# Optimization experiments

Measured on AMD Instinct MI355X. Metric: run time of the kernel, lower is better.

The kernel has to match this reference:

```python
import jax, jax.numpy as jnp
import numpy as np
from jax import lax

B, TENC, TMEL = 32, 512, 400
E, H, A, P, M, F, K = 512, 512, 512, 256, 128, 32, 31


def setup_inputs() -> dict:
    key = jax.random.key(0)
    ks = jax.random.split(key, 20)
    def rn(i, shape, fan_in):
        return jax.random.normal(ks[i], shape, jnp.float32) / np.float32(np.sqrt(fan_in))
    return dict(
        enc_outputs=jax.random.normal(ks[0], (B, TENC, 2 * E), jnp.float32),
        mel_spec_true=jax.random.normal(ks[1], (B, TMEL, M), jnp.float32),
        text_lens=jax.random.randint(ks[2], (B,), 0, TENC),
        mel_spec_lens=jax.random.randint(ks[3], (B,), 0, TMEL),
        max_text_len=TENC,
        pre_w1=rn(4, (M, P), M), pre_w2=rn(5, (P, P), P),
        attn_wi=rn(6, (P + E, 3 * H), P + E), attn_wh=rn(7, (H, 3 * H), H),
        attn_bi=jnp.zeros((3 * H,), jnp.float32), attn_bh=jnp.zeros((3 * H,), jnp.float32),
        q_w=rn(8, (H, A), H), k_w=rn(9, (2 * E, A), 2 * E),
        score_w=rn(10, (A, 1), A), score_b=jnp.zeros((1,), jnp.float32),
        loc_conv_w=rn(11, (F, 2, K), 2 * K), loc_w=rn(12, (F, A), F), loc_b=jnp.zeros((A,), jnp.float32),
        out_wi=rn(13, (A + H, 3 * H), A + H), out_wh=rn(14, (H, 3 * H), H),
        out_bi=jnp.zeros((3 * H,), jnp.float32), out_bh=jnp.zeros((3 * H,), jnp.float32),
        dec_w=rn(15, (H + A, M), H + A), dec_b=jnp.zeros((M,), jnp.float32),
        gate_w=rn(16, (H + A, 1), H + A), gate_b=jnp.zeros((1,), jnp.float32),
    )


def _gru_step(x, h, wi, wh, bi, bh):
    # single-step torch nn.GRU cell; gate order r, z, n
    gi = x @ wi + bi
    gh = h @ wh + bh
    ir, iz, inn = jnp.split(gi, 3, axis=-1)
    hr, hz, hn = jnp.split(gh, 3, axis=-1)
    r = jax.nn.sigmoid(ir + hr)
    z = jax.nn.sigmoid(iz + hz)
    n = jnp.tanh(inn + r * hn)
    return (1.0 - z) * n + z * h


def reference(enc_outputs, mel_spec_true, text_lens, mel_spec_lens, max_text_len,
              pre_w1, pre_w2, attn_wi, attn_wh, attn_bi, attn_bh,
              q_w, k_w, score_w, score_b, loc_conv_w, loc_w, loc_b,
              out_wi, out_wh, out_bi, out_bh, dec_w, dec_b, gate_w, gate_b):
    Bsz, Tenc, _ = enc_outputs.shape
    Tmel = mel_spec_true.shape[1]
    Hd = attn_wh.shape[0]
    Ad = k_w.shape[1]
    pad = (loc_conv_w.shape[2] - 1) // 2

    keys_p = enc_outputs @ k_w                                # [B,Tenc,A]
    enc_mask = jnp.arange(Tenc)[None, :] > text_lens[:, None]  # True = masked (t > len)

    def prenet(x):  # dropout disabled for determinism
        return jax.nn.relu(jax.nn.relu(x @ pre_w1) @ pre_w2)

    dec_in0 = prenet(jnp.zeros((Bsz, mel_spec_true.shape[2]), enc_outputs.dtype))
    carry0 = (jnp.zeros((Bsz, Hd), jnp.float32), jnp.zeros((Bsz, Hd), jnp.float32),
              jnp.zeros((Bsz, Tenc), jnp.float32), jnp.zeros((Bsz, Tenc), jnp.float32),
              jnp.zeros((Bsz, Ad), jnp.float32), dec_in0)

    def step(carry, _):
        h_attn, h_out, att_w, att_cum, ctx, dec_in = carry
        h_attn = _gru_step(jnp.concatenate([dec_in, ctx], -1), h_attn, attn_wi, attn_wh, attn_bi, attn_bh)
        loc_in = jnp.stack([att_w, att_cum], axis=1)           # [B,2,Tenc]
        loc = lax.conv_general_dilated(loc_in, loc_conv_w, (1,), [(pad, pad)],
                                       dimension_numbers=('NCH', 'OIH', 'NCH'))  # [B,F,Tenc]
        loc = jnp.swapaxes(loc, 1, 2) @ loc_w + loc_b          # [B,Tenc,A]
        q = (h_attn @ q_w)[:, None, :]                         # [B,1,A]
        s = (jnp.tanh(q + keys_p + loc) @ score_w + score_b)[..., 0]  # [B,Tenc]
        s = jnp.where(enc_mask, -jnp.inf, s)
        att_w = jax.nn.softmax(s, axis=1)
        ctx = jnp.einsum('bt,bta->ba', att_w, keys_p)
        att_cum = att_cum + att_w
        h_out = _gru_step(jnp.concatenate([h_attn, ctx], -1), h_out, out_wi, out_wh, out_bi, out_bh)
        att_h = jnp.concatenate([h_out, ctx], -1)
        mel = att_h @ dec_w + dec_b                            # [B,M]
        stop = (att_h @ gate_w + gate_b)[:, 0]                 # [B]
        dec_in = prenet(mel)                                   # teacher_force_ratio = 0
        return (h_attn, h_out, att_w, att_cum, ctx, dec_in), (mel, stop, att_w)

    _, (mels, gates, attns) = lax.scan(step, carry0, None, length=Tmel)
    mels = jnp.swapaxes(mels, 0, 1)    # [B,Tmel,M]
    gates = jnp.swapaxes(gates, 0, 1)  # [B,Tmel]
    attns = jnp.swapaxes(attns, 0, 1)  # [B,Tmel,Tenc]
    mel_mask = jnp.arange(Tmel)[None, :] > mel_spec_lens[:, None]
    masked_mel = jnp.where(mel_mask[:, :, None], 0.0, mels)
    masked_gate = jnp.where(mel_mask, 1000.0, gates)
    return masked_mel, masked_gate, attns, mel_mask
```

## Files before the change

### kernel.cpp

```cpp
#include <hip/hip_runtime.h>
#include <hip/hip_fp16.h>
#include <math.h>

#define NBLK 256
#define NTHR 1024

__device__ __forceinline__ float fast_rcp(float x) {
#if __has_builtin(__builtin_amdgcn_rcpf)
  return __builtin_amdgcn_rcpf(x);
#else
  return 1.f / x;
#endif
}
__device__ __forceinline__ float fast_sigmoid(float x) { return fast_rcp(1.f + __expf(-x)); }
__device__ __forceinline__ float fast_tanh(float x) { return 1.f - 2.f * fast_rcp(1.f + __expf(2.f * x)); }

union HU2 { unsigned int u; __half2 h; };
union HU4 { uint4 u; __half2 h[4]; };
__device__ __forceinline__ float2 cvt2(unsigned int u) { HU2 t; t.u = u; return __half22float2(t.h); }

__device__ __forceinline__ void sta(float* p, float v) {
  __hip_atomic_store(p, v, __ATOMIC_RELAXED, __HIP_MEMORY_SCOPE_AGENT);
}
__device__ __forceinline__ float lda(const float* p) {
  return __hip_atomic_load(p, __ATOMIC_RELAXED, __HIP_MEMORY_SCOPE_AGENT);
}
__device__ __forceinline__ int ldai(const int* p) {
  return __hip_atomic_load(p, __ATOMIC_RELAXED, __HIP_MEMORY_SCOPE_AGENT);
}
__device__ __forceinline__ void ntst(float* p, float v) { __builtin_nontemporal_store(v, p); }

struct Params {
  const float *enc, *pre_w1, *pre_w2, *attn_bi, *attn_bh;
  const float *q_w, *k_w, *score_w, *score_b, *conv_w, *loc_w, *loc_b;
  const float *out_bi, *out_bh, *dec_b, *gate_b;
  const float *attn_wi, *attn_wh, *out_wi, *out_wh, *dec_w, *gate_w;
  const int *text_lens, *mel_lens;
  __half *hkeys, *gw1T, *gw2T, *decT, *pre1T, *pre2T, *gateh, *locwh, *qwT;
  float *hA, *hO, *attw, *attcum, *decin, *ebuf, *zpart, *ctxacc, *ctxacc2, *stateZ;
  int *done, *zdone, *done2, *hAdone;
  unsigned *barc;
  float *out_mel, *out_gate, *out_attn, *out_mask;
};

__global__ __launch_bounds__(512) void k_keys(Params p) {
  __shared__ float sA[16][132];
  __shared__ float sB[16][68];
  int tid = threadIdx.x;
  int row0 = blockIdx.x * 128, col0 = blockIdx.y * 64;
  float acc[4][4] = {};
  int r = tid >> 2, kq = tid & 3;
  int tx = tid & 15, ty = tid >> 4;
  for (int k0 = 0; k0 < 1024; k0 += 16) {
    __syncthreads();
    float4 a4 = *(const float4*)(p.enc + (size_t)(row0 + r) * 1024 + k0 + kq * 4);
    sA[kq * 4 + 0][r] = a4.x; sA[kq * 4 + 1][r] = a4.y;
    sA[kq * 4 + 2][r] = a4.z; sA[kq * 4 + 3][r] = a4.w;
    if (tid < 256) {
      int kb = tid >> 4, nb = (tid & 15) * 4;
      float4 b4 = *(const float4*)(p.k_w + (size_t)(k0 + kb) * 512 + col0 + nb);
      sB[kb][nb + 0] = b4.x; sB[kb][nb + 1] = b4.y;
      sB[kb][nb + 2] = b4.z; sB[kb][nb + 3] = b4.w;
    }
    __syncthreads();
#pragma unroll
    for (int k = 0; k < 16; k++) {
      float ar[4], br[4];
#pragma unroll
      for (int i = 0; i < 4; i++) { ar[i] = sA[k][ty * 4 + i]; br[i] = sB[k][tx * 4 + i]; }
#pragma unroll
      for (int i = 0; i < 4; i++)
#pragma unroll
        for (int j = 0; j < 4; j++) acc[i][j] = fmaf(ar[i], br[j], acc[i][j]);
    }
  }
#pragma unroll
  for (int i = 0; i < 4; i++)
#pragma unroll
    for (int j = 0; j < 4; j++)
      p.hkeys[(size_t)(row0 + ty * 4 + i) * 512 + col0 + tx * 4 + j] = __float2half(acc[i][j]);
}

__global__ __launch_bounds__(256) void k_repack(Params p) {
  const int gsz = gridDim.x * 256;
  const int t0 = blockIdx.x * 256 + threadIdx.x;
  for (int i = t0; i < 1280 * 512; i += gsz) {
    int r = i >> 9, u = i & 511;
    const float* src = (r < 768) ? p.attn_wi + (size_t)r * 1536 : p.attn_wh + (size_t)(r - 768) * 1536;
    __half2* d = (__half2*)(p.gw1T + ((size_t)i << 2));
    d[0] = __halves2half2(__float2half(src[u]), __float2half(src[512 + u]));
    d[1] = __halves2half2(__float2half(src[1024 + u]), __float2half(0.f));
  }
  for (int i = t0; i < 1536 * 512; i += gsz) {
    int r = i >> 9, u = i & 511;
    const float* src = (r < 1024) ? p.out_wi + (size_t)r * 1536 : p.out_wh + (size_t)(r - 1024) * 1536;
    __half2* d = (__half2*)(p.gw2T + ((size_t)i << 2));
    d[0] = __halves2half2(__float2half(src[u]), __float2half(src[512 + u]));
    d[1] = __halves2half2(__float2half(src[1024 + u]), __float2half(0.f));
  }
  for (int i = t0; i < 512 * 512; i += gsz) {
    int k = i >> 9, a = i & 511;
    p.qwT[(size_t)a * 512 + k] = __float2half(p.q_w[(size_t)k * 512 + a]);
  }
  for (int i = t0; i < 1024 * 128; i += gsz) {
    int k = i >> 7, m = i & 127;
    p.decT[(size_t)m * 1024 + k] = __float2half(p.dec_w[(size_t)k * 128 + m]);
  }
  for (int i = t0; i < 1024; i += gsz) p.gateh[i] = __float2half(p.gate_w[i]);
  for (int i = t0; i < 16384; i += gsz) p.locwh[i] = __float2half(p.loc_w[i]);
  for (int i = t0; i < 128 * 256; i += gsz) {
    int m = i >> 8, pc = i & 255;
    p.pre1T[(size_t)pc * 128 + m] = __float2half(p.pre_w1[(size_t)m * 256 + pc]);
  }
  for (int i = t0; i < 256 * 256; i += gsz) {
    int k = i >> 8, pc = i & 255;
    p.pre2T[(size_t)pc * 256 + k] = __float2half(p.pre_w2[(size_t)k * 256 + pc]);
  }
  for (int i = t0; i < 106496; i += gsz) p.stateZ[i] = 0.f;
  for (int i = t0; i < 16384; i += gsz) p.ctxacc[i] = 0.f;
  for (int i = t0; i < 16384; i += gsz) p.ctxacc2[i] = 0.f;
  for (int i = t0; i < 512; i += gsz) p.barc[i] = 0u;
  for (int i = t0; i < 2048; i += gsz) p.zdone[i] = 0;
  for (int i = t0; i < 12800; i += gsz) {
    int b = i / 400, t = i - b * 400;
    p.out_mask[i] = (t > p.mel_lens[b]) ? 1.f : 0.f;
  }
}

struct SMemMega {
  __half keysL[64 * 512];
  float ctxL[4][512];
  float invZ[4];
  union {
    struct { float x[4][1544]; float4 part4[16][64]; } gr;
    struct { float locS[64][33]; float aw[94]; float ac[94]; float hA_s[512]; float qS[512];
             float qpart[2][512]; float cpred[8][512]; float eS[64]; } s3;
    struct { float xh[1024]; float red[1024]; float mel[128]; float p1[256]; } s6;
  } u;
};

__device__ __forceinline__ void gchunk(const uint2* __restrict__ w,
                                       const float* __restrict__ x, int ks,
                                       int j0, int j1,
                                       float& a0, float& a1, float& a2) {
#pragma unroll 8
  for (int j = j0; j < j1; ++j) {
    uint2 wv = w[(size_t)j << 13];
    float xv = x[ks + (j << 4)];
    float2 f0 = cvt2(wv.x);
    float nf = cvt2(wv.y).x;
    a0 = fmaf(xv, f0.x, a0);
    a1 = fmaf(xv, f0.y, a1);
    a2 = fmaf(xv, nf, a2);
  }
}

__global__ __launch_bounds__(NTHR) void mega(Params p) {
  __shared__ SMemMega sm;
  const int blk = blockIdx.x, tid = threadIdx.x;
  const int ug = blk & 31, bg = blk >> 5, b0 = bg * 4;
  const int bS = blk & 31, t8 = blk >> 5, t0g = t8 << 6;

  const int u_ = tid & 15, b2_ = (tid >> 4) & 3, ks_ = tid >> 6;
  const int uG_ = (ug << 4) + u_;
  const uint2* w1 = (const uint2*)p.gw1T + ((size_t)ks_ << 9) + uG_;
  const uint2* w2 = (const uint2*)p.gw2T + ((size_t)ks_ << 9) + uG_;

  {
    const uint4* src = (const uint4*)(p.hkeys + (((size_t)(bS << 9) + t0g) << 9));
    uint4* dst = (uint4*)sm.keysL;
    for (int i = tid; i < 4096; i += NTHR) dst[i] = src[i];
    for (int i = tid; i < 2048; i += NTHR) sm.ctxL[i >> 9][i & 511] = 0.f;
  }
  __syncthreads();

  float g1r = 0.f, g1z = 0.f, g1ni = 0.f, g1nh = 0.f;

#pragma clang loop unroll(disable)
  for (int step = 0; step < 400; step++) {
    const int par = step & 1;
    float* hA_prev = p.hA + par * 16384;
    float* hA_next = p.hA + (par ^ 1) * 16384;
    float* hO_prev = p.hO + par * 16384;
    float* hO_next = p.hO + (par ^ 1) * 16384;
    float* cCur = par ? p.ctxacc2 : p.ctxacc;
    float* cNxt = par ? p.ctxacc : p.ctxacc2;

    {
      if (step > 0) {
        if (tid < 4) {
          while (ldai(&p.done2[(b0 + tid) * 16]) < 4 * step)
            __builtin_amdgcn_s_sleep(2);
        }
        __syncthreads();
      }
      for (int i = tid; i < 1024; i += NTHR)
        sm.u.gr.x[i >> 8][i & 255] = lda(&p.decin[((b0 + (i >> 8)) << 8) + (i & 255)]);
      __syncthreads();
      gchunk(w1, &sm.u.gr.x[b2_][0], ks_, 0, 16, g1r, g1z, g1ni);
      sm.u.gr.part4[ks_][(u_ << 2) + b2_] = make_float4(g1r, g1z, g1ni, g1nh);
      __syncthreads();
      if (tid < 64) {
        int uu = tid >> 2, bb2 = tid & 3;
        float4 s = make_float4(0.f, 0.f, 0.f, 0.f);
#pragma unroll
        for (int l = 0; l < 16; l++) {
          float4 v = sm.u.gr.part4[l][(uu << 2) + bb2];
          s.x += v.x; s.y += v.y; s.z += v.z; s.w += v.w;
        }
        int uGf = (ug << 4) + uu;
        float r = fast_sigmoid(s.x + p.attn_bi[uGf] + p.attn_bh[uGf]);
        float z = fast_sigmoid(s.y + p.attn_bi[512 + uGf] + p.attn_bh[512 + uGf]);
        float n = fast_tanh(s.z + p.attn_bi[1024 + uGf] + r * (s.w + p.attn_bh[1024 + uGf]));
        float hv = lda(&hA_prev[((b0 + bb2) << 9) + uGf]);
        sta(&hA_next[((b0 + bb2) << 9) + uGf], (1.f - z) * n + z * hv);
      }
      asm volatile("s_waitcnt vmcnt(0)" ::: "memory");
      if (tid < 4) atomicAdd(&p.hAdone[(b0 + tid) * 16], 1);
    }

    {
      if (tid == 0) {
        while (ldai(&p.hAdone[bS * 16]) < 32 * (step + 1))
          __builtin_amdgcn_s_sleep(2);
      }
      __syncthreads();
      if (t8 == 0) {
        for (int i = tid; i < 512; i += NTHR) sta(&cNxt[(bS << 9) + i], 0.f);
      }
      const int tlen = p.text_lens[bS];
      for (int j = tid; j < 94; j += NTHR) {
        int pp = t0g - 15 + j;
        bool ok = (unsigned)pp < 512u;
        sm.u.s3.aw[j] = ok ? lda(&p.attw[(bS << 9) + pp]) : 0.f;
        sm.u.s3.ac[j] = ok ? lda(&p.attcum[(bS << 9) + pp]) : 0.f;
      }
      if (tid < 512) sm.u.s3.hA_s[tid] = lda(&hA_next[(bS << 9) + tid]);
      __syncthreads();
      for (int i = tid; i < 2048; i += NTHR) {
        int tt = i >> 5, f = i & 31;
        const float* w0 = p.conv_w + f * 62;
        float a = 0.f;
#pragma unroll
        for (int k = 0; k < 31; k++)
          a = fmaf(w0[k], sm.u.s3.aw[tt + k], fmaf(w0[31 + k], sm.u.s3.ac[tt + k], a));
        sm.u.s3.locS[tt][f] = a;
      }
      {
        int a = tid & 511, ks = tid >> 9;
        const HU4* qp = (const HU4*)(p.qwT + (size_t)a * 512 + ks * 256);
        float q0 = 0.f, q1 = 0.f;
#pragma unroll 4
        for (int it = 0; it < 32; it++) {
          HU4 raw = qp[it];
          int kb = ks * 256 + it * 8;
#pragma unroll
          for (int h2 = 0; h2 < 4; h2++) {
            float2 w = __half22float2(raw.h[h2]);
            q0 = fmaf(sm.u.s3.hA_s[kb + h2 * 2], w.x, q0);
            q1 = fmaf(sm.u.s3.hA_s[kb + h2 * 2 + 1], w.y, q1);
          }
        }
        sm.u.s3.qpart[ks][a] = q0 + q1;
      }
      __syncthreads();
      if (tid < 512)
        sm.u.s3.qS[tid] = sm.u.s3.qpart[0][tid] + sm.u.s3.qpart[1][tid] + p.loc_b[tid];
      __syncthreads();
      const int lane = tid & 63, wv = tid >> 6;
      float acc[4][8];
      float4 qA = *(const float4*)&sm.u.s3.qS[lane * 8];
      float4 qB = *(const float4*)&sm.u.s3.qS[lane * 8 + 4];
#pragma unroll
      for (int j = 0; j < 4; j++) {
        int tL = wv * 4 + j;
        HU4 raw; raw.u = *(const uint4*)&sm.keysL[tL * 512 + lane * 8];
        float2 k0 = __half22float2(raw.h[0]), k1 = __half22float2(raw.h[1]);
        float2 k2 = __half22float2(raw.h[2]), k3 = __half22float2(raw.h[3]);
        acc[j][0] = qA.x + k0.x; acc[j][1] = qA.y + k0.y;
        acc[j][2] = qA.z + k1.x; acc[j][3] = qA.w + k1.y;
        acc[j][4] = qB.x + k2.x; acc[j][5] = qB.y + k2.y;
        acc[j][6] = qB.z + k3.x; acc[j][7] = qB.w + k3.y;
      }
#pragma unroll 4
      for (int f = 0; f < 32; f++) {
        HU4 rw; rw.u = *(const uint4*)(p.locwh + (size_t)f * 512 + lane * 8);
        float2 w0 = __half22float2(rw.h[0]), w1 = __half22float2(rw.h[1]);
        float2 w2 = __half22float2(rw.h[2]), w3 = __half22float2(rw.h[3]);
#pragma unroll
        for (int j = 0; j < 4; j++) {
          float lf = sm.u.s3.locS[wv * 4 + j][f];
          acc[j][0] = fmaf(lf, w0.x, acc[j][0]); acc[j][1] = fmaf(lf, w0.y, acc[j][1]);
          acc[j][2] = fmaf(lf, w1.x, acc[j][2]); acc[j][3] = fmaf(lf, w1.y, acc[j][3]);
          acc[j][4] = fmaf(lf, w2.x, acc[j][4]); acc[j][5] = fmaf(lf, w2.y, acc[j][5]);
          acc[j][6] = fmaf(lf, w3.x, acc[j][6]); acc[j][7] = fmaf(lf, w3.y, acc[j][7]);
        }
      }
      float4 sA = *(const float4*)(p.score_w + lane * 8);
      float4 sB = *(const float4*)(p.score_w + lane * 8 + 4);
      float sbias = p.score_b[0];
      float e_reg[4];
#pragma unroll
      for (int j = 0; j < 4; j++) {
        float pv = fast_tanh(acc[j][0]) * sA.x + fast_tanh(acc[j][1]) * sA.y +
                   fast_tanh(acc[j][2]) * sA.z + fast_tanh(acc[j][3]) * sA.w +
                   fast_tanh(acc[j][4]) * sB.x + fast_tanh(acc[j][5]) * sB.y +
                   fast_tanh(acc[j][6]) * sB.z + fast_tanh(acc[j][7]) * sB.w;
#pragma unroll
        for (int off = 32; off > 0; off >>= 1) pv += __shfl_xor(pv, off, 64);
        int t = t0g + wv * 4 + j;
        e_reg[j] = (t > tlen) ? 0.f : __expf(pv + sbias);
      }
      if (lane == 0) {
#pragma unroll
        for (int j = 0; j < 4; j++) sm.u.s3.eS[wv * 4 + j] = e_reg[j];
      }
      float cp[8] = {0.f, 0.f, 0.f, 0.f, 0.f, 0.f, 0.f, 0.f};
#pragma unroll
      for (int j = 0; j < 4; j++) {
        int tL = wv * 4 + j;
        HU4 raw; raw.u = *(const uint4*)&sm.keysL[tL * 512 + lane * 8];
        float2 k0 = __half22float2(raw.h[0]), k1 = __half22float2(raw.h[1]);
        float2 k2 = __half22float2(raw.h[2]), k3 = __half22float2(raw.h[3]);
        float e = e_reg[j];
        cp[0] = fmaf(e, k0.x, cp[0]); cp[1] = fmaf(e, k0.y, cp[1]);
        cp[2] = fmaf(e, k1.x, cp[2]); cp[3] = fmaf(e, k1.y, cp[3]);
        cp[4] = fmaf(e, k2.x, cp[4]); cp[5] = fmaf(e, k2.y, cp[5]);
        cp[6] = fmaf(e, k3.x, cp[6]); cp[7] = fmaf(e, k3.y, cp[7]);
      }
      __syncthreads();
      if (wv < 8) {
        float4* r0 = (float4*)&sm.u.s3.cpred[wv][lane * 8];
        r0[0] = make_float4(cp[0], cp[1], cp[2], cp[3]);
        r0[1] = make_float4(cp[4], cp[5], cp[6], cp[7]);
      }
      __syncthreads();
      if (wv >= 8) {
        float* r0 = &sm.u.s3.cpred[wv - 8][lane * 8];
#pragma unroll
        for (int i = 0; i < 8; i++) r0[i] += cp[i];
      }
      __syncthreads();
      if (tid < 512) {
        float s = 0.f;
#pragma unroll
        for (int j = 0; j < 8; j++) s += sm.u.s3.cpred[j][tid];
        atomicAdd(&cCur[(bS << 9) + tid], s);
      }
      if (tid < 64) {
        float e = sm.u.s3.eS[tid];
        sta(&p.ebuf[(bS << 9) + t0g + tid], e);
        float z = e;
#pragma unroll
        for (int off = 32; off > 0; off >>= 1) z += __shfl_xor(z, off, 64);
        if (tid == 0) sta(&p.zpart[bS * 8 + t8], z);
      }
      if (tid < 512 && (tid & 63) == 0) {
        asm volatile("s_waitcnt vmcnt(0)" ::: "memory");
        atomicAdd(&p.zdone[bS * 16], 1);
      }
    }

    {
      if (tid < 4) {
        while (ldai(&p.zdone[(b0 + tid) * 16]) < 64 * (step + 1))
          __builtin_amdgcn_s_sleep(2);
        float Z = 0.f;
#pragma unroll
        for (int j = 0; j < 8; j++) Z += lda(&p.zpart[(b0 + tid) * 8 + j]);
        sm.invZ[tid] = fast_rcp(Z);
      }
      __syncthreads();
      for (int i = tid; i < 2048; i += NTHR) {
        int b2 = i >> 9, a = i & 511;
        sm.ctxL[b2][a] = lda(&cCur[((b0 + b2) << 9) + a]) * sm.invZ[b2];
      }
      if (ug == 0) {
        for (int i = tid; i < 2048; i += NTHR) {
          int b2 = i >> 9, t = i & 511;
          int bb = b0 + b2;
          float v = lda(&p.ebuf[(bb << 9) + t]) * sm.invZ[b2];
          sta(&p.attw[(bb << 9) + t], v);
          float oc = lda(&p.attcum[(bb << 9) + t]);
          sta(&p.attcum[(bb << 9) + t], oc + v);
          ntst(&p.out_attn[(size_t)bb * 204800 + (size_t)step * 512 + t], v);
        }
      }
      __syncthreads();
      for (int i = tid; i < 2048; i += NTHR) {
        int b2 = i >> 9, a = i & 511;
        sm.u.gr.x[b2][a] = lda(&hA_next[((b0 + b2) << 9) + a]);
      }
      for (int i = tid; i < 2048; i += NTHR) {
        int b2 = i >> 9, a = i & 511;
        sm.u.gr.x[b2][512 + a] = sm.ctxL[b2][a];
      }
      for (int i = tid; i < 2048; i += NTHR) {
        int b2 = i >> 9, a = i & 511;
        sm.u.gr.x[b2][1024 + a] = lda(&hO_prev[((b0 + b2) << 9) + a]);
      }
      __syncthreads();
      {
        float r2 = 0.f, z2 = 0.f, ni2 = 0.f, nh2 = 0.f;
        gchunk(w2, &sm.u.gr.x[b2_][0], ks_, 0, 64, r2, z2, ni2);
        gchunk(w2, &sm.u.gr.x[b2_][0], ks_, 64, 96, r2, z2, nh2);
        sm.u.gr.part4[ks_][(u_ << 2) + b2_] = make_float4(r2, z2, ni2, nh2);
      }
      __syncthreads();
      if (tid < 64) {
        int uu = tid >> 2, bb2 = tid & 3;
        float4 s = make_float4(0.f, 0.f, 0.f, 0.f);
#pragma unroll
        for (int l = 0; l < 16; l++) {
          float4 v = sm.u.gr.part4[l][(uu << 2) + bb2];
          s.x += v.x; s.y += v.y; s.z += v.z; s.w += v.w;
        }
        int uGf = (ug << 4) + uu;
        float r = fast_sigmoid(s.x + p.out_bi[uGf] + p.out_bh[uGf]);
        float z = fast_sigmoid(s.y + p.out_bi[512 + uGf] + p.out_bh[512 + uGf]);
        float n = fast_tanh(s.z + p.out_bi[1024 + uGf] + r * (s.w + p.out_bh[1024 + uGf]));
        float hv = sm.u.gr.x[bb2][1024 + uGf];
        sta(&hO_next[((b0 + bb2) << 9) + uGf], (1.f - z) * n + z * hv);
      }
      asm volatile("s_waitcnt vmcnt(0)" ::: "memory");
      if (tid < 4) atomicAdd(&p.done[(b0 + tid) * 16], 1);
      g1r = 0.f; g1z = 0.f; g1ni = 0.f; g1nh = 0.f;
      if (step < 399) {
        gchunk(w1, &sm.u.gr.x[b2_][0] + 256, ks_, 16, 48, g1r, g1z, g1ni);
        gchunk(w1, &sm.u.gr.x[b2_][0] - 768, ks_, 48, 80, g1r, g1z, g1nh);
      }
      if (ug < 4) {
        const int bb = b0 + ug;
        if (tid == 0) {
          int target = 32 * (step + 1);
          while (ldai(&p.done[bb * 16]) < target)
            __builtin_amdgcn_s_sleep(2);
        }
        __syncthreads();
        sm.u.s6.xh[tid] = (tid < 512) ? lda(&hO_next[(bb << 9) + tid])
                                      : sm.ctxL[ug][tid - 512];
        __syncthreads();
        bool masked = step > p.mel_lens[bb];
        {
          int m = tid & 127, ks = tid >> 7;
          const HU4* dp = (const HU4*)(p.decT + (size_t)m * 1024 + ks * 128);
          float a = 0.f;
#pragma unroll 4
          for (int it = 0; it < 16; it++) {
            HU4 raw = dp[it];
            int kb = ks * 128 + it * 8;
#pragma unroll
            for (int h2 = 0; h2 < 4; h2++) {
              float2 w = __half22float2(raw.h[h2]);
              a = fmaf(sm.u.s6.xh[kb + h2 * 2], w.x, a);
              a = fmaf(sm.u.s6.xh[kb + h2 * 2 + 1], w.y, a);
            }
          }
          sm.u.s6.red[tid] = a;
        }
        __syncthreads();
        if (tid < 128) {
          float mv = p.dec_b[tid];
#pragma unroll
          for (int j = 0; j < 8; j++) mv += sm.u.s6.red[tid + j * 128];
          sm.u.s6.mel[tid] = mv;
          ntst(&p.out_mel[(size_t)bb * 51200 + (size_t)step * 128 + tid], masked ? 0.f : mv);
        }
        __syncthreads();
        sm.u.s6.red[tid] = sm.u.s6.xh[tid] * __half2float(p.gateh[tid]);
        __syncthreads();
        if (tid < 64) {
          float g = 0.f;
#pragma unroll
          for (int j = 0; j < 16; j++) g += sm.u.s6.red[tid + j * 64];
#pragma unroll
          for (int off = 32; off > 0; off >>= 1) g += __shfl_xor(g, off, 64);
          if (tid == 0) ntst(&p.out_gate[bb * 400 + step], masked ? 1000.f : (g + p.gate_b[0]));
        }
        __syncthreads();
        {
          int pc = tid & 255, ks = tid >> 8;
          const HU4* wp = (const HU4*)(p.pre1T + (size_t)pc * 128 + ks * 32);
          float a = 0.f;
#pragma unroll
          for (int it = 0; it < 4; it++) {
            HU4 raw = wp[it];
            int kb = ks * 32 + it * 8;
#pragma unroll
            for (int h2 = 0; h2 < 4; h2++) {
              float2 w = __half22float2(raw.h[h2]);
              a = fmaf(sm.u.s6.mel[kb + h2 * 2], w.x, a);
              a = fmaf(sm.u.s6.mel[kb + h2 * 2 + 1], w.y, a);
            }
          }
          sm.u.s6.red[tid] = a;
        }
        __syncthreads();
        if (tid < 256) {
          float a = sm.u.s6.red[tid] + sm.u.s6.red[tid + 256] +
                    sm.u.s6.red[tid + 512] + sm.u.s6.red[tid + 768];
          sm.u.s6.p1[tid] = fmaxf(a, 0.f);
        }
        __syncthreads();
        {
          int pc = tid & 255, ks = tid >> 8;
          const HU4* wp = (const HU4*)(p.pre2T + (size_t)pc * 256 + ks * 64);
          float a = 0.f;
#pragma unroll
          for (int it = 0; it < 8; it++) {
            HU4 raw = wp[it];
            int kb = ks * 64 + it * 8;
#pragma unroll
            for (int h2 = 0; h2 < 4; h2++) {
              float2 w = __half22float2(raw.h[h2]);
              a = fmaf(sm.u.s6.p1[kb + h2 * 2], w.x, a);
              a = fmaf(sm.u.s6.p1[kb + h2 * 2 + 1], w.y, a);
            }
          }
          sm.u.s6.red[tid] = a;
        }
        __syncthreads();
        if (tid < 256) {
          float a = sm.u.s6.red[tid] + sm.u.s6.red[tid + 256] +
                    sm.u.s6.red[tid + 512] + sm.u.s6.red[tid + 768];
          sta(&p.decin[(bb << 8) + tid], fmaxf(a, 0.f));
        }
        if (tid < 256 && (tid & 63) == 0) {
          asm volatile("s_waitcnt vmcnt(0)" ::: "memory");
          atomicAdd(&p.done2[bb * 16], 1);
        }
      }
    }
  }
}

extern "C" void kernel_launch(void* const* d_in, const int* in_sizes, int n_in,
                              void* d_out, int out_size, void* d_ws, size_t ws_size,
                              hipStream_t stream) {
  Params p;
  p.enc       = (const float*)d_in[0];
  p.text_lens = (const int*)d_in[2];
  p.mel_lens  = (const int*)d_in[3];
  p.pre_w1    = (const float*)d_in[5];
  p.pre_w2    = (const float*)d_in[6];
  p.attn_wi   = (const float*)d_in[7];
  p.attn_wh   = (const float*)d_in[8];
  p.attn_bi   = (const float*)d_in[9];
  p.attn_bh   = (const float*)d_in[10];
  p.q_w       = (const float*)d_in[11];
  p.k_w       = (const float*)d_in[12];
  p.score_w   = (const float*)d_in[13];
  p.score_b   = (const float*)d_in[14];
  p.conv_w    = (const float*)d_in[15];
  p.loc_w     = (const float*)d_in[16];
  p.loc_b     = (const float*)d_in[17];
  p.out_wi    = (const float*)d_in[18];
  p.out_wh    = (const float*)d_in[19];
  p.out_bi    = (const float*)d_in[20];
  p.out_bh    = (const float*)d_in[21];
  p.dec_w     = (const float*)d_in[22];
  p.dec_b     = (const float*)d_in[23];
  p.gate_w    = (const float*)d_in[24];
  p.gate_b    = (const float*)d_in[25];

  float* ws = (float*)d_ws;
  p.hkeys  = (__half*)(ws);
  p.gw1T   = (__half*)(ws + 4194304);
  p.gw2T   = (__half*)(ws + 5505024);
  p.decT   = (__half*)(ws + 7077888);
  p.pre1T  = (__half*)(ws + 7143424);
  p.pre2T  = (__half*)(ws + 7159808);
  p.gateh  = (__half*)(ws + 7192576);
  p.locwh  = (__half*)(ws + 7193088);
  p.qwT    = (__half*)(ws + 7201280);
  p.hA     = ws + 7332352;
  p.hO     = ws + 7365120;
  p.attw   = ws + 7397888;
  p.attcum = ws + 7414272;
  p.decin  = ws + 7430656;
  p.stateZ = p.hA;
  p.ebuf   = ws + 7438848;
  p.zpart  = ws + 7455232;
  p.ctxacc = ws + 7455488;
  p.done   = (int*)(ws + 7490336);
  p.barc   = (unsigned*)(ws + 7471904);
  p.ctxacc2 = ws + 7472416;
  p.zdone  = (int*)(ws + 7488800);
  p.done2  = (int*)(ws + 7489312);
  p.hAdone = (int*)(ws + 7489824);
  float* out = (float*)d_out;
  p.out_mel  = out;
  p.out_gate = out + 1638400;
  p.out_attn = out + 1651200;
  p.out_mask = out + 8204800;

  k_repack<<<2048, 256, 0, stream>>>(p);
  k_keys<<<dim3(128, 8), 512, 0, stream>>>(p);
  void* args[] = { (void*)&p };
  hipLaunchCooperativeKernel((const void*)mega, dim3(NBLK), dim3(NTHR), args, 0, stream);
}
```

Measured before the change: 43.72 ms.

## Split query projection across blocks and overlap output-GRU matvec chunks with attention

The query projection is now split so each block computes only its 64-column slice, publishes it to a global qbuf, and signals a new qdone counter; blocks then wait and gather the full query. The location conv is moved after that publish to hide the wait. The output-GRU hidden-state and attention-hidden chunks of the w2 matvec are computed early in dedicated shared buffers (hO2, hA2) instead of all at once after the context is ready. This shortens the critical path per step, at the cost of an extra cross-block sync and more shared memory.

```diff
diff --git a/kernel.cpp b/kernel.cpp
--- a/kernel.cpp
+++ b/kernel.cpp
@@ -38,8 +38,8 @@
   const int *text_lens, *mel_lens;
   __half *hkeys, *gw1T, *gw2T, *decT, *pre1T, *pre2T, *gateh, *locwh, *qwT;
   float *hA, *hO, *attw, *attcum, *decin, *ebuf, *zpart, *ctxacc, *ctxacc2, *stateZ;
-  int *done, *zdone, *done2, *hAdone;
-  unsigned *barc;
+  float *qbuf;
+  int *done, *zdone, *done2, *hAdone, *qdone;
   float *out_mel, *out_gate, *out_attn, *out_mask;
 };
 
@@ -119,7 +119,7 @@
   for (int i = t0; i < 106496; i += gsz) p.stateZ[i] = 0.f;
   for (int i = t0; i < 16384; i += gsz) p.ctxacc[i] = 0.f;
   for (int i = t0; i < 16384; i += gsz) p.ctxacc2[i] = 0.f;
-  for (int i = t0; i < 512; i += gsz) p.barc[i] = 0u;
+  for (int i = t0; i < 512; i += gsz) p.qdone[i] = 0;
   for (int i = t0; i < 2048; i += gsz) p.zdone[i] = 0;
   for (int i = t0; i < 12800; i += gsz) {
     int b = i / 400, t = i - b * 400;
@@ -129,12 +129,14 @@
 
 struct SMemMega {
   __half keysL[64 * 512];
-  float ctxL[4][512];
+  float ctxL[4][520];
+  float hA2[4][520];
+  float hO2[4][520];
   float invZ[4];
   union {
-    struct { float x[4][1544]; float4 part4[16][64]; } gr;
-    struct { float locS[64][33]; float aw[94]; float ac[94]; float hA_s[512]; float qS[512];
-             float qpart[2][512]; float cpred[8][512]; float eS[64]; } s3;
+    struct { float x[4][264]; float4 part4[16][64]; } gr;
+    struct { float locS[64][33]; float aw[94]; float ac[94]; float hA_s[512];
+             float qS[512]; float qp2[16][64]; float cpred[8][512]; float eS[64]; } s3;
     struct { float xh[1024]; float red[1024]; float mel[128]; float p1[256]; } s6;
   } u;
 };
@@ -186,6 +188,8 @@
     float* cCur = par ? p.ctxacc2 : p.ctxacc;
     float* cNxt = par ? p.ctxacc : p.ctxacc2;
 
+    float r2 = 0.f, z2 = 0.f, ni2 = 0.f, nh2 = 0.f;
+
     {
       if (step > 0) {
         if (tid < 4) {
@@ -196,6 +200,8 @@
       }
       for (int i = tid; i < 1024; i += NTHR)
         sm.u.gr.x[i >> 8][i & 255] = lda(&p.decin[((b0 + (i >> 8)) << 8) + (i & 255)]);
+      for (int i = tid; i < 2048; i += NTHR)
+        sm.hO2[i >> 9][i & 511] = lda(&hO_prev[((b0 + (i >> 9)) << 9) + (i & 511)]);
       __syncthreads();
       gchunk(w1, &sm.u.gr.x[b2_][0], ks_, 0, 16, g1r, g1z, g1ni);
       sm.u.gr.part4[ks_][(u_ << 2) + b2_] = make_float4(g1r, g1z, g1ni, g1nh);
@@ -217,43 +223,34 @@
       }
       asm volatile("s_waitcnt vmcnt(0)" ::: "memory");
       if (tid < 4) atomicAdd(&p.hAdone[(b0 + tid) * 16], 1);
+      gchunk(w2, &sm.hO2[b2_][0] - 1024, ks_, 64, 96, r2, z2, nh2);
     }
 
     {
-      if (tid == 0) {
-        while (ldai(&p.hAdone[bS * 16]) < 32 * (step + 1))
-          __builtin_amdgcn_s_sleep(2);
-      }
-      __syncthreads();
-      if (t8 == 0) {
-        for (int i = tid; i < 512; i += NTHR) sta(&cNxt[(bS << 9) + i], 0.f);
-      }
-      const int tlen = p.text_lens[bS];
       for (int j = tid; j < 94; j += NTHR) {
         int pp = t0g - 15 + j;
         bool ok = (unsigned)pp < 512u;
         sm.u.s3.aw[j] = ok ? lda(&p.attw[(bS << 9) + pp]) : 0.f;
         sm.u.s3.ac[j] = ok ? lda(&p.attcum[(bS << 9) + pp]) : 0.f;
       }
+      if (tid == 0) {
+        while (ldai(&p.hAdone[bS * 16]) < 32 * (step + 1))
+          __builtin_amdgcn_s_sleep(2);
+      }
+      __syncthreads();
+      if (t8 == 0) {
+        for (int i = tid; i < 512; i += NTHR) sta(&cNxt[(bS << 9) + i], 0.f);
+      }
       if (tid < 512) sm.u.s3.hA_s[tid] = lda(&hA_next[(bS << 9) + tid]);
       __syncthreads();
-      for (int i = tid; i < 2048; i += NTHR) {
-        int tt = i >> 5, f = i & 31;
-        const float* w0 = p.conv_w + f * 62;
-        float a = 0.f;
-#pragma unroll
-        for (int k = 0; k < 31; k++)
-          a = fmaf(w0[k], sm.u.s3.aw[tt + k], fmaf(w0[31 + k], sm.u.s3.ac[tt + k], a));
-        sm.u.s3.locS[tt][f] = a;
-      }
       {
-        int a = tid & 511, ks = tid >> 9;
-        const HU4* qp = (const HU4*)(p.qwT + (size_t)a * 512 + ks * 256);
+        int a = tid & 63, ks = tid >> 6;
+        const HU4* qp = (const HU4*)(p.qwT + (size_t)(t0g + a) * 512 + ks * 32);
         float q0 = 0.f, q1 = 0.f;
-#pragma unroll 4
-        for (int it = 0; it < 32; it++) {
+#pragma unroll
+        for (int it = 0; it < 4; it++) {
           HU4 raw = qp[it];
-          int kb = ks * 256 + it * 8;
+          int kb = ks * 32 + it * 8;
 #pragma unroll
           for (int h2 = 0; h2 < 4; h2++) {
             float2 w = __half22float2(raw.h[h2]);
@@ -261,11 +258,35 @@
             q1 = fmaf(sm.u.s3.hA_s[kb + h2 * 2 + 1], w.y, q1);
           }
         }
-        sm.u.s3.qpart[ks][a] = q0 + q1;
-      }
-      __syncthreads();
-      if (tid < 512)
-        sm.u.s3.qS[tid] = sm.u.s3.qpart[0][tid] + sm.u.s3.qpart[1][tid] + p.loc_b[tid];
+        sm.u.s3.qp2[ks][a] = q0 + q1;
+      }
+      __syncthreads();
+      if (tid < 64) {
+        float s = 0.f;
+#pragma unroll
+        for (int l = 0; l < 16; l++) s += sm.u.s3.qp2[l][tid];
+        sta(&p.qbuf[(bS << 9) + t0g + tid], s + p.loc_b[t0g + tid]);
+      }
+      if (tid == 0) {
+        asm volatile("s_waitcnt vmcnt(0)" ::: "memory");
+        atomicAdd(&p.qdone[bS * 16], 1);
+      }
+      const int tlen = p.text_lens[bS];
+      for (int i = tid; i < 2048; i += NTHR) {
+        int tt = i >> 5, f = i & 31;
+        const float* w0 = p.conv_w + f * 62;
+        float a = 0.f;
+#pragma unroll
+        for (int k = 0; k < 31; k++)
+          a = fmaf(w0[k], sm.u.s3.aw[tt + k], fmaf(w0[31 + k], sm.u.s3.ac[tt + k], a));
+        sm.u.s3.locS[tt][f] = a;
+      }
+      if (tid == 0) {
+        while (ldai(&p.qdone[bS * 16]) < 8 * (step + 1))
+          __builtin_amdgcn_s_sleep(2);
+      }
+      __syncthreads();
+      if (tid < 512) sm.u.s3.qS[tid] = lda(&p.qbuf[(bS << 9) + tid]);
       __syncthreads();
       const int lane = tid & 63, wv = tid >> 6;
       float acc[4][8];
@@ -286,13 +307,13 @@
       for (int f = 0; f < 32; f++) {
         HU4 rw; rw.u = *(const uint4*)(p.locwh + (size_t)f * 512 + lane * 8);
         float2 w0 = __half22float2(rw.h[0]), w1 = __half22float2(rw.h[1]);
-        float2 w2 = __half22float2(rw.h[2]), w3 = __half22float2(rw.h[3]);
+        float2 w2v = __half22float2(rw.h[2]), w3 = __half22float2(rw.h[3]);
 #pragma unroll
         for (int j = 0; j < 4; j++) {
           float lf = sm.u.s3.locS[wv * 4 + j][f];
           acc[j][0] = fmaf(lf, w0.x, acc[j][0]); acc[j][1] = fmaf(lf, w0.y, acc[j][1]);
           acc[j][2] = fmaf(lf, w1.x, acc[j][2]); acc[j][3] = fmaf(lf, w1.y, acc[j][3]);
-          acc[j][4] = fmaf(lf, w2.x, acc[j][4]); acc[j][5] = fmaf(lf, w2.y, acc[j][5]);
+          acc[j][4] = fmaf(lf, w2v.x, acc[j][4]); acc[j][5] = fmaf(lf, w2v.y, acc[j][5]);
           acc[j][6] = fmaf(lf, w3.x, acc[j][6]); acc[j][7] = fmaf(lf, w3.y, acc[j][7]);
         }
       }
@@ -359,6 +380,15 @@
         asm volatile("s_waitcnt vmcnt(0)" ::: "memory");
         atomicAdd(&p.zdone[bS * 16], 1);
       }
+      if (tid < 4) {
+        while (ldai(&p.hAdone[(b0 + tid) * 16]) < 32 * (step + 1))
+          __builtin_amdgcn_s_sleep(2);
+      }
+      __syncthreads();
+      for (int i = tid; i < 2048; i += NTHR)
+        sm.hA2[i >> 9][i & 511] = lda(&hA_next[((b0 + (i >> 9)) << 9) + (i & 511)]);
+      __syncthreads();
+      gchunk(w2, &sm.hA2[b2_][0], ks_, 0, 32, r2, z2, ni2);
     }
 
     {
@@ -375,37 +405,19 @@
         int b2 = i >> 9, a = i & 511;
         sm.ctxL[b2][a] = lda(&cCur[((b0 + b2) << 9) + a]) * sm.invZ[b2];
       }
-      if (ug == 0) {
-        for (int i = tid; i < 2048; i += NTHR) {
-          int b2 = i >> 9, t = i & 511;
-          int bb = b0 + b2;
-          float v = lda(&p.ebuf[(bb << 9) + t]) * sm.invZ[b2];
-          sta(&p.attw[(bb << 9) + t], v);
-          float oc = lda(&p.attcum[(bb << 9) + t]);
-          sta(&p.attcum[(bb << 9) + t], oc + v);
-          ntst(&p.out_attn[(size_t)bb * 204800 + (size_t)step * 512 + t], v);
-        }
-      }
-      __syncthreads();
-      for (int i = tid; i < 2048; i += NTHR) {
-        int b2 = i >> 9, a = i & 511;
-        sm.u.gr.x[b2][a] = lda(&hA_next[((b0 + b2) << 9) + a]);
-      }
-      for (int i = tid; i < 2048; i += NTHR) {
-        int b2 = i >> 9, a = i & 511;
-        sm.u.gr.x[b2][512 + a] = sm.ctxL[b2][a];
-      }
-      for (int i = tid; i < 2048; i += NTHR) {
-        int b2 = i >> 9, a = i & 511;
-        sm.u.gr.x[b2][1024 + a] = lda(&hO_prev[((b0 + b2) << 9) + a]);
-      }
-      __syncthreads();
-      {
-        float r2 = 0.f, z2 = 0.f, ni2 = 0.f, nh2 = 0.f;
-        gchunk(w2, &sm.u.gr.x[b2_][0], ks_, 0, 64, r2, z2, ni2);
-        gchunk(w2, &sm.u.gr.x[b2_][0], ks_, 64, 96, r2, z2, nh2);
-        sm.u.gr.part4[ks_][(u_ << 2) + b2_] = make_float4(r2, z2, ni2, nh2);
-      }
+      if (ug < 4) {
+        const int bb = b0 + ug;
+        if (tid < 512) {
+          float v = lda(&p.ebuf[(bb << 9) + tid]) * sm.invZ[ug];
+          sta(&p.attw[(bb << 9) + tid], v);
+          float oc = lda(&p.attcum[(bb << 9) + tid]);
+          sta(&p.attcum[(bb << 9) + tid], oc + v);
+          ntst(&p.out_attn[(size_t)bb * 204800 + (size_t)step * 512 + tid], v);
+        }
+      }
+      __syncthreads();
+      gchunk(w2, &sm.ctxL[b2_][0] - 512, ks_, 32, 64, r2, z2, ni2);
+      sm.u.gr.part4[ks_][(u_ << 2) + b2_] = make_float4(r2, z2, ni2, nh2);
       __syncthreads();
       if (tid < 64) {
         int uu = tid >> 2, bb2 = tid & 3;
@@ -419,16 +431,11 @@
         float r = fast_sigmoid(s.x + p.out_bi[uGf] + p.out_bh[uGf]);
         float z = fast_sigmoid(s.y + p.out_bi[512 + uGf] + p.out_bh[512 + uGf]);
         float n = fast_tanh(s.z + p.out_bi[1024 + uGf] + r * (s.w + p.out_bh[1024 + uGf]));
-        float hv = sm.u.gr.x[bb2][1024 + uGf];
+        float hv = sm.hO2[bb2][uGf];
         sta(&hO_next[((b0 + bb2) << 9) + uGf], (1.f - z) * n + z * hv);
       }
       asm volatile("s_waitcnt vmcnt(0)" ::: "memory");
       if (tid < 4) atomicAdd(&p.done[(b0 + tid) * 16], 1);
-      g1r = 0.f; g1z = 0.f; g1ni = 0.f; g1nh = 0.f;
-      if (step < 399) {
-        gchunk(w1, &sm.u.gr.x[b2_][0] + 256, ks_, 16, 48, g1r, g1z, g1ni);
-        gchunk(w1, &sm.u.gr.x[b2_][0] - 768, ks_, 48, 80, g1r, g1z, g1nh);
-      }
       if (ug < 4) {
         const int bb = b0 + ug;
         if (tid == 0) {
@@ -529,6 +536,11 @@
           asm volatile("s_waitcnt vmcnt(0)" ::: "memory");
           atomicAdd(&p.done2[bb * 16], 1);
         }
+      }
+      g1r = 0.f; g1z = 0.f; g1ni = 0.f; g1nh = 0.f;
+      if (step < 399) {
+        gchunk(w1, &sm.ctxL[b2_][0] - 256, ks_, 16, 48, g1r, g1z, g1ni);
+        gchunk(w1, &sm.hA2[b2_][0] - 768, ks_, 48, 80, g1r, g1z, g1nh);
       }
     }
   }
@@ -582,12 +594,13 @@
   p.ebuf   = ws + 7438848;
   p.zpart  = ws + 7455232;
   p.ctxacc = ws + 7455488;
-  p.done   = (int*)(ws + 7490336);
-  p.barc   = (unsigned*)(ws + 7471904);
+  p.qdone  = (int*)(ws + 7471904);
   p.ctxacc2 = ws + 7472416;
   p.zdone  = (int*)(ws + 7488800);
   p.done2  = (int*)(ws + 7489312);
   p.hAdone = (int*)(ws + 7489824);
+  p.done   = (int*)(ws + 7490336);
+  p.qbuf   = ws + 7490848;
   float* out = (float*)d_out;
   p.out_mel  = out;
   p.out_gate = out + 1638400;
```

Result: faster. 37.60 ms, median of 2 (-14.0%).
